# Optimization experiments

Measured on AMD Instinct MI355X. Metric: run time of the kernel, lower is better.

The kernel has to match this reference:

```python
import jax, jax.numpy as jnp
import numpy as np

N, E, D = 50000, 800000, 128
RESIDUAL_SCALE = 1.0
EPS = 1e-5  # torch LayerNorm default eps


def _mlp_ln(h, w1, b1, w2, b2, w3, b3, g, beta):
    # MeshGraphNets MLP: Linear -> SiLU -> Linear -> SiLU -> Linear -> LayerNorm
    h = jax.nn.silu(h @ w1 + b1)
    h = jax.nn.silu(h @ w2 + b2)
    h = h @ w3 + b3
    mu = h.mean(axis=-1, keepdims=True)
    var = ((h - mu) ** 2).mean(axis=-1, keepdims=True)
    return g * (h - mu) * jax.lax.rsqrt(var + EPS) + beta


def setup_inputs() -> dict:
    key = jax.random.key(0)
    ks = jax.random.split(key, 16)

    def lin(k, fan_in, fan_out):
        bound = 1.0 / np.sqrt(fan_in)
        kw, kb = jax.random.split(k)
        w = jax.random.uniform(kw, (fan_in, fan_out), jnp.float32, -bound, bound)
        b = jax.random.uniform(kb, (fan_out,), jnp.float32, -bound, bound)
        return w, b

    x = jax.random.normal(ks[0], (N, D), jnp.float32)
    edge_attr = jax.random.normal(ks[1], (E, D), jnp.float32)
    edge_index = jax.random.randint(ks[2], (2, E), 0, N, jnp.int32)

    ew1, eb1 = lin(ks[3], 3 * D, D)
    ew2, eb2 = lin(ks[4], D, D)
    ew3, eb3 = lin(ks[5], D, D)
    e_gamma = jnp.ones((D,), jnp.float32)
    e_beta = jnp.zeros((D,), jnp.float32)

    nw1, nb1 = lin(ks[6], 2 * D, D)
    nw2, nb2 = lin(ks[7], D, D)
    nw3, nb3 = lin(ks[8], D, D)
    n_gamma = jnp.ones((D,), jnp.float32)
    n_beta = jnp.zeros((D,), jnp.float32)

    return dict(x=x, edge_attr=edge_attr, edge_index=edge_index,
                ew1=ew1, eb1=eb1, ew2=ew2, eb2=eb2, ew3=ew3, eb3=eb3,
                e_gamma=e_gamma, e_beta=e_beta,
                nw1=nw1, nb1=nb1, nw2=nw2, nb2=nb2, nw3=nw3, nb3=nb3,
                n_gamma=n_gamma, n_beta=n_beta)


def reference(x, edge_attr, edge_index,
              ew1, eb1, ew2, eb2, ew3, eb3, e_gamma, e_beta,
              nw1, nb1, nw2, nb2, nw3, nb3, n_gamma, n_beta):
    senders, receivers = edge_index[0], edge_index[1]

    # EdgeBlock: gather endpoint node features, concat with edge_attr, MLP
    edge_in = jnp.concatenate([x[senders], x[receivers], edge_attr], axis=-1)  # [E, 3D]
    edge_mlp_out = _mlp_ln(edge_in, ew1, eb1, ew2, eb2, ew3, eb3, e_gamma, e_beta)  # [E, D]

    # NodeBlock: scatter-sum edge messages to receiver nodes, concat with x, MLP
    agg = jax.ops.segment_sum(edge_mlp_out, receivers, num_segments=N)  # [N, D]
    node_in = jnp.concatenate([x, agg], axis=-1)  # [N, 2D]
    node_mlp_out = _mlp_ln(node_in, nw1, nb1, nw2, nb2, nw3, nb3, n_gamma, n_beta)

    # Residual updates
    x_new = x + RESIDUAL_SCALE * node_mlp_out

    # PairNorm (use_pairnorm=True)
    x_centered = x_new - x_new.mean(axis=0, keepdims=True)
    rms = jnp.linalg.norm(x_centered) / jnp.sqrt(jnp.float32(x_new.shape[0])) + 1e-8
    x_new = x_centered / rms

    edge_attr_new = edge_attr + RESIDUAL_SCALE * edge_mlp_out
    return x_new, edge_attr_new
```

## Files before the change

### kernel.cpp

```cpp
#include <hip/hip_runtime.h>
#include <hip/hip_bf16.h>

#define NN 50000
#define NE 800000
#define ROWB 272

typedef unsigned short u16;
typedef unsigned int u32;
typedef __attribute__((ext_vector_type(4))) float f32x4;
typedef __attribute__((ext_vector_type(8))) short short8;


__device__ __forceinline__ u16 f2b(float f){ __hip_bfloat16 h = __float2bfloat16(f); u16 u; __builtin_memcpy(&u, &h, 2); return u; }
__device__ __forceinline__ float b2f(u16 u){ __hip_bfloat16 h; __builtin_memcpy(&h, &u, 2); return __bfloat162float(h); }
__device__ __forceinline__ float siluf(float v){ return v / (1.f + __expf(-v)); }

__device__ __forceinline__ uint4 cvt8(const float* __restrict__ s){
  const float4 a = *(const float4*)s;
  const float4 b = *(const float4*)(s + 4);
  union { u16 h[8]; uint4 q; } u;
  u.h[0]=f2b(a.x); u.h[1]=f2b(a.y); u.h[2]=f2b(a.z); u.h[3]=f2b(a.w);
  u.h[4]=f2b(b.x); u.h[5]=f2b(b.y); u.h[6]=f2b(b.z); u.h[7]=f2b(b.w);
  return u.q;
}

template<int K>
__device__ __forceinline__ void gemm128(f32x4 acc[4][2], const u16* __restrict__ sA,
                                        const u16* __restrict__ wB, int wm, int wn, int lane){
  const int l15 = lane & 15, l4 = lane >> 4;
  const u16* w0 = wB + (size_t)(wn*32 + l15)*K + l4*8;
  const u16* w1 = w0 + (size_t)16*K;
  #pragma unroll
  for (int ks = 0; ks < 4; ++ks){
    const short8 b0 = *(const short8*)(w0 + ks*32);
    const short8 b1 = *(const short8*)(w1 + ks*32);
    const int kb = ks*64 + l4*16;
    short8 a[4];
    #pragma unroll
    for (int fr = 0; fr < 4; ++fr)
      a[fr] = *(const short8*)((const char*)sA + (wm*64 + fr*16 + l15)*ROWB + kb);
    #pragma unroll
    for (int fr = 0; fr < 4; ++fr){
      acc[fr][0] = __builtin_amdgcn_mfma_f32_16x16x32_bf16(a[fr], b0, acc[fr][0], 0, 0, 0);
      acc[fr][1] = __builtin_amdgcn_mfma_f32_16x16x32_bf16(a[fr], b1, acc[fr][1], 0, 0, 0);
    }
  }
}

template<int K>
__device__ __forceinline__ void gemm64(f32x4 acc[2][4], const u16* __restrict__ sA,
                                       const u16* __restrict__ wB, int wm, int wn, int lane){
  const int l15 = lane & 15, l4 = lane >> 4;
  const u16* w0 = wB + (size_t)(wn*64 + l15)*K + l4*8;
  #pragma unroll
  for (int ks = 0; ks < 4; ++ks){
    short8 b[4];
    #pragma unroll
    for (int fc = 0; fc < 4; ++fc)
      b[fc] = *(const short8*)(w0 + (size_t)fc*16*K + ks*32);
    const int kb = ks*64 + l4*16;
    short8 a[2];
    #pragma unroll
    for (int fr = 0; fr < 2; ++fr)
      a[fr] = *(const short8*)((const char*)sA + (wm*32 + fr*16 + l15)*ROWB + kb);
    #pragma unroll
    for (int fr = 0; fr < 2; ++fr)
      #pragma unroll
      for (int fc = 0; fc < 4; ++fc)
        acc[fr][fc] = __builtin_amdgcn_mfma_f32_16x16x32_bf16(a[fr], b[fc], acc[fr][fc], 0, 0, 0);
  }
}

__device__ __forceinline__ void epilogue(const f32x4 acc[4][2], const float* __restrict__ bias,
                                         u16* __restrict__ dst, int wm, int wn, int lane, bool doSilu){
  const int l15 = lane & 15, l4 = lane >> 4;
  #pragma unroll
  for (int fc = 0; fc < 2; ++fc){
    const int col = wn*32 + fc*16 + l15;
    const float bv = bias[col];
    #pragma unroll
    for (int fr = 0; fr < 4; ++fr){
      const int rbase = wm*64 + fr*16 + l4*4;
      #pragma unroll
      for (int j = 0; j < 4; ++j){
        float v = acc[fr][fc][j] + bv;
        if (doSilu) v = siluf(v);
        *(u16*)((char*)dst + (rbase + j)*ROWB + col*2) = f2b(v);
      }
    }
  }
}

__global__ __launch_bounds__(256) void wtrans_kernel(const float* __restrict__ w1, const float* __restrict__ w2,
                                                     const float* __restrict__ w3, const float* __restrict__ m1,
                                                     const float* __restrict__ m2, const float* __restrict__ m3,
                                                     u16* __restrict__ wt){
  const int i = blockIdx.x * 256 + threadIdx.x;
  const float* src; int K, base, off;
  if      (i < 49152)  { src = w1; K = 384; base = 0;      off = i; }
  else if (i < 65536)  { src = w2; K = 128; base = 49152;  off = i - 49152; }
  else if (i < 81920)  { src = w3; K = 128; base = 65536;  off = i - 65536; }
  else if (i < 114688) { src = m1; K = 256; base = 81920;  off = i - 81920; }
  else if (i < 131072) { src = m2; K = 128; base = 114688; off = i - 114688; }
  else                 { src = m3; K = 128; base = 131072; off = i - 131072; }
  const int k = off >> 7, n = off & 127;
  wt[base + n*K + k] = f2b(src[off]);
}

__global__ __launch_bounds__(256) void prep_kernel(const float* __restrict__ x, u16* __restrict__ xB,
                                                   const int* __restrict__ eidx, int* __restrict__ cnt){
  const int i = blockIdx.x * 256 + threadIdx.x;
  if (xB){
    const size_t o = (size_t)i * 8;
    *(uint4*)(xB + o) = cvt8(x + o);
  }
  atomicAdd(&cnt[eidx[NE + i]], 1);
}

__global__ __launch_bounds__(1024) void scan_kernel(const int* __restrict__ cnt, int* __restrict__ off,
                                                    int* __restrict__ cursor){
  __shared__ int s[1024];
  const int t = threadIdx.x;
  const int CH = 49;
  int sum = 0;
  for (int i = 0; i < CH; ++i){
    const int idx = t*CH + i;
    if (idx < NN) sum += cnt[idx];
  }
  s[t] = sum;
  __syncthreads();
  for (int d = 1; d < 1024; d <<= 1){
    int v = (t >= d) ? s[t - d] : 0;
    __syncthreads();
    s[t] += v;
    __syncthreads();
  }
  int run = s[t] - sum;
  for (int i = 0; i < CH; ++i){
    const int idx = t*CH + i;
    if (idx < NN){
      off[idx] = run;
      cursor[idx] = run;
      run += cnt[idx];
      if (idx == NN - 1) off[NN] = run;
    }
  }
}

__global__ __launch_bounds__(256) void scatter_kernel(const int* __restrict__ eidx, int* __restrict__ cursor,
                                                      int* __restrict__ perm, int* __restrict__ slot){
  const int i = blockIdx.x * 256 + threadIdx.x;
  if (i < NE){
    const int pos = atomicAdd(&cursor[eidx[NE + i]], 1);
    perm[pos] = i;
    slot[i] = pos;
  }
}

__global__ __launch_bounds__(256, 4) void pre_kernel(const float* __restrict__ x, const u16* __restrict__ xB,
                                                     const u16* __restrict__ wt, u16* __restrict__ Pab){
  __shared__ u16 sX[64*136];
  const int t = threadIdx.x;
  const int nBase = blockIdx.x * 64;
  const int lane = t & 63, wid = t >> 6;
  const int wm = wid >> 1, wn = wid & 1;
  const int chunk = t & 15, r0 = t >> 4;

  #pragma unroll
  for (int p = 0; p < 4; ++p){
    const int row = r0 + p*16;
    const int node = nBase + row;
    uint4 v = {0u, 0u, 0u, 0u};
    if (node < NN){
      if (xB) v = *(const uint4*)(xB + (size_t)node*128 + chunk*8);
      else    v = cvt8(x + (size_t)node*128 + chunk*8);
    }
    *(uint4*)((char*)sX + row*ROWB + chunk*16) = v;
  }
  __syncthreads();

  const f32x4 z4 = {0.f, 0.f, 0.f, 0.f};
  const int l15 = lane & 15, l4 = lane >> 4;
  #pragma unroll
  for (int half = 0; half < 2; ++half){
    f32x4 acc[2][4];
    #pragma unroll
    for (int fr = 0; fr < 2; ++fr)
      #pragma unroll
      for (int fc = 0; fc < 4; ++fc) acc[fr][fc] = z4;
    gemm64<384>(acc, sX, wt + half*128, wm, wn, lane);
    #pragma unroll
    for (int fc = 0; fc < 4; ++fc){
      const int col = wn*64 + fc*16 + l15;
      #pragma unroll
      for (int fr = 0; fr < 2; ++fr){
        const int rbase = wm*32 + fr*16 + l4*4;
        #pragma unroll
        for (int j = 0; j < 4; ++j){
          const int node = nBase + rbase + j;
          if (node < NN) Pab[(size_t)node*256 + half*128 + col] = f2b(acc[fr][fc][j]);
        }
      }
    }
  }
}

__global__ __launch_bounds__(512, 4) void edge_kernel(
    const float* __restrict__ x, const u16* __restrict__ xB,
    const float* __restrict__ ea, const int* __restrict__ eidx,
    const u16* __restrict__ wt, const u16* __restrict__ Pab,
    const float* __restrict__ b1, const float* __restrict__ b2,
    const float* __restrict__ b3, const float* __restrict__ gma, const float* __restrict__ bta,
    const int* __restrict__ slot, float* __restrict__ outE, u16* __restrict__ oBuf)
{
  __shared__ u16 sA[128*136];
  __shared__ u16 sP[128*128];
  __shared__ float sMeta[640];
  __shared__ int sIdx[256];
  __shared__ int sSlot[128];
  const int t = threadIdx.x;
  const size_t eBase = (size_t)blockIdx.x * 128;

  if (t < 128){
    sIdx[t]       = eidx[eBase + t];
    sIdx[t + 128] = eidx[(size_t)NE + eBase + t];
    sSlot[t]      = slot[eBase + t];
    sMeta[t]       = b1[t];
    sMeta[t + 128] = b2[t];
    sMeta[t + 256] = b3[t];
    sMeta[t + 384] = gma[t];
    sMeta[t + 512] = bta[t];
  }
  __syncthreads();

  const int lane = t & 63, wid = t >> 6;
  const int wm = wid >> 2, wn = wid & 3;
  const int chunk = t & 15, r0 = t >> 4;

  const f32x4 z4 = {0.f, 0.f, 0.f, 0.f};
  f32x4 acc[4][2];
  #pragma unroll
  for (int fr = 0; fr < 4; ++fr){ acc[fr][0] = z4; acc[fr][1] = z4; }

  uint4 eaQ[4];

  #pragma unroll
  for (int p = 0; p < 4; ++p){
    const int row = r0 + p*32;
    uint4 v = cvt8(ea + ((eBase + row)*128 + chunk*8));
    eaQ[p] = v;
    *(uint4*)((char*)sA + row*ROWB + chunk*16) = v;
    const int sn = sIdx[row], rn = sIdx[row + 128];
    const uint4 qa = *(const uint4*)(Pab + (size_t)sn*256 + chunk*8);
    const uint4 qb = *(const uint4*)(Pab + (size_t)rn*256 + 128 + chunk*8);
    const u16* pa = (const u16*)&qa;
    const u16* pb = (const u16*)&qb;
    union { u16 h[8]; uint4 q; } u;
    #pragma unroll
    for (int j = 0; j < 8; ++j) u.h[j] = f2b(b2f(pa[j]) + b2f(pb[j]));
    *(uint4*)((char*)sP + row*256 + chunk*16) = u.q;
  }
  __syncthreads();
  gemm128<384>(acc, sA, wt + 256, wm, wn, lane);
  __syncthreads();

  {
    const int l15 = lane & 15, l4 = lane >> 4;
    #pragma unroll
    for (int fc = 0; fc < 2; ++fc){
      const int col = wn*32 + fc*16 + l15;
      const float bv = sMeta[col];
      #pragma unroll
      for (int fr = 0; fr < 4; ++fr){
        const int rbase = wm*64 + fr*16 + l4*4;
        #pragma unroll
        for (int j = 0; j < 4; ++j){
          const float pv = b2f(*(const u16*)((const char*)sP + (rbase + j)*256 + col*2));
          const float v = siluf(acc[fr][fc][j] + bv + pv);
          *(u16*)((char*)sA + (rbase + j)*ROWB + col*2) = f2b(v);
        }
      }
    }
  }
  __syncthreads();
  #pragma unroll
  for (int fr = 0; fr < 4; ++fr){ acc[fr][0] = z4; acc[fr][1] = z4; }
  gemm128<128>(acc, sA, wt + 49152, wm, wn, lane);
  __syncthreads();
  epilogue(acc, sMeta + 128, sA, wm, wn, lane, true);
  __syncthreads();
  #pragma unroll
  for (int fr = 0; fr < 4; ++fr){ acc[fr][0] = z4; acc[fr][1] = z4; }
  gemm128<128>(acc, sA, wt + 65536, wm, wn, lane);
  __syncthreads();
  epilogue(acc, sMeta + 256, sA, wm, wn, lane, false);
  __syncthreads();

  {
    #pragma unroll
    for (int p = 0; p < 4; ++p){
      const int row = r0 + p*32;
      uint4 q = *(const uint4*)((const char*)sA + row*ROWB + chunk*16);
      const u16* pu = (const u16*)&q;
      float h[8];
      #pragma unroll
      for (int j = 0; j < 8; ++j) h[j] = b2f(pu[j]);
      float s = 0.f;
      #pragma unroll
      for (int j = 0; j < 8; ++j) s += h[j];
      s += __shfl_xor(s, 1); s += __shfl_xor(s, 2); s += __shfl_xor(s, 4); s += __shfl_xor(s, 8);
      const float mu = s * (1.f/128.f);
      float ss = 0.f;
      #pragma unroll
      for (int j = 0; j < 8; ++j){ const float d = h[j] - mu; ss += d*d; }
      ss += __shfl_xor(ss, 1); ss += __shfl_xor(ss, 2); ss += __shfl_xor(ss, 4); ss += __shfl_xor(ss, 8);
      const float rs = rsqrtf(fmaxf(ss*(1.f/128.f), 0.f) + 1e-5f);
      const size_t e = eBase + row;
      const u16* ep = (const u16*)&eaQ[p];
      alignas(16) float orow[8];
      alignas(16) u16 obf[8];
      #pragma unroll
      for (int j = 0; j < 8; ++j){
        const int col = chunk*8 + j;
        const float o = sMeta[384 + col]*(h[j] - mu)*rs + sMeta[512 + col];
        orow[j] = b2f(ep[j]) + o;
        obf[j] = f2b(o);
      }
      float* dst = outE + e*128 + chunk*8;
      *(float4*)dst       = ((const float4*)orow)[0];
      *(float4*)(dst + 4) = ((const float4*)orow)[1];
      if (oBuf) *(uint4*)(oBuf + (size_t)sSlot[row]*128 + chunk*8) = *(const uint4*)obf;
    }
  }
}

__global__ __launch_bounds__(256) void agg_o_kernel(const u16* __restrict__ oBuf, const int* __restrict__ off,
                                                    float* __restrict__ agg){
  const int node = blockIdx.x * 4 + (threadIdx.x >> 6);
  const int lane = threadIdx.x & 63;
  if (node >= NN) return;
  const int s = off[node], e = off[node + 1];
  float a0 = 0.f, a1 = 0.f;
  for (int i = s; i < e; ++i){
    const u32 w = *(const u32*)(oBuf + (size_t)i*128 + lane*2);
    a0 += b2f((u16)(w & 0xFFFFu));
    a1 += b2f((u16)(w >> 16));
  }
  float2 r = {a0, a1};
  *(float2*)(agg + (size_t)node*128 + lane*2) = r;
}

__global__ __launch_bounds__(256) void agg_f_kernel(const float* __restrict__ outE, const float* __restrict__ ea,
                                                    const int* __restrict__ off, const int* __restrict__ perm,
                                                    float* __restrict__ agg){
  const int node = blockIdx.x * 4 + (threadIdx.x >> 6);
  const int lane = threadIdx.x & 63;
  if (node >= NN) return;
  const int s = off[node], e = off[node + 1];
  float a0 = 0.f, a1 = 0.f;
  for (int i = s; i < e; ++i){
    const size_t r = (size_t)perm[i] * 128;
    a0 += outE[r + lane]      - ea[r + lane];
    a1 += outE[r + 64 + lane] - ea[r + 64 + lane];
  }
  agg[(size_t)node*128 + lane]      = a0;
  agg[(size_t)node*128 + 64 + lane] = a1;
}

__global__ __launch_bounds__(512, 4) void node_kernel(
    const float* __restrict__ x, const float* __restrict__ agg, const u16* __restrict__ wt,
    const float* __restrict__ b1, const float* __restrict__ b2, const float* __restrict__ b3,
    const float* __restrict__ gma, const float* __restrict__ bta,
    float* __restrict__ outX, float* __restrict__ stats)
{
  __shared__ u16 sA[128*136];
  __shared__ float sMeta[640];
  __shared__ float sCol[128];
  __shared__ float sSq;
  const int t = threadIdx.x;
  const int nBase = blockIdx.x * 128;

  if (t < 128){
    sMeta[t]       = b1[t];
    sMeta[t + 128] = b2[t];
    sMeta[t + 256] = b3[t];
    sMeta[t + 384] = gma[t];
    sMeta[t + 512] = bta[t];
    sCol[t] = 0.f;
  }
  if (t == 0) sSq = 0.f;
  __syncthreads();

  const int lane = t & 63, wid = t >> 6;
  const int wm = wid >> 2, wn = wid & 3;
  const int chunk = t & 15, r0 = t >> 4;

  const f32x4 z4 = {0.f, 0.f, 0.f, 0.f};
  f32x4 acc[4][2];
  #pragma unroll
  for (int fr = 0; fr < 4; ++fr){ acc[fr][0] = z4; acc[fr][1] = z4; }

  for (int kc = 0; kc < 2; ++kc){
    #pragma unroll
    for (int p = 0; p < 4; ++p){
      const int row = r0 + p*32;
      const int node = nBase + row;
      uint4 v = {0u, 0u, 0u, 0u};
      if (node < NN){
        const float* s = (kc == 0) ? (x + (size_t)node*128 + chunk*8)
                                   : (agg + (size_t)node*128 + chunk*8);
        v = cvt8(s);
      }
      *(uint4*)((char*)sA + row*ROWB + chunk*16) = v;
    }
    __syncthreads();
    gemm128<256>(acc, sA, wt + 81920 + kc*128, wm, wn, lane);
    __syncthreads();
  }
  epilogue(acc, sMeta + 0, sA, wm, wn, lane, true);
  __syncthreads();
  #pragma unroll
  for (int fr = 0; fr < 4; ++fr){ acc[fr][0] = z4; acc[fr][1] = z4; }
  gemm128<128>(acc, sA, wt + 114688, wm, wn, lane);
  __syncthreads();
  epilogue(acc, sMeta + 128, sA, wm, wn, lane, true);
  __syncthreads();
  #pragma unroll
  for (int fr = 0; fr < 4; ++fr){ acc[fr][0] = z4; acc[fr][1] = z4; }
  gemm128<128>(acc, sA, wt + 131072, wm, wn, lane);
  __syncthreads();
  epilogue(acc, sMeta + 256, sA, wm, wn, lane, false);
  __syncthreads();

  {
    const int row = t >> 2, part = t & 3;
    const int node = nBase + row;
    float v[32];
    #pragma unroll
    for (int c = 0; c < 4; ++c){
      uint4 q = *(const uint4*)((const char*)sA + row*ROWB + part*64 + c*16);
      const u16* pu = (const u16*)&q;
      #pragma unroll
      for (int j = 0; j < 8; ++j) v[c*8 + j] = b2f(pu[j]);
    }
    float s = 0.f;
    #pragma unroll
    for (int i = 0; i < 32; ++i) s += v[i];
    s += __shfl_xor(s, 1);  s += __shfl_xor(s, 2);
    const float mu = s * (1.f/128.f);
    float ss = 0.f;
    #pragma unroll
    for (int i = 0; i < 32; ++i){ const float d = v[i] - mu; ss += d*d; }
    ss += __shfl_xor(ss, 1);  ss += __shfl_xor(ss, 2);
    const float rs = rsqrtf(fmaxf(ss*(1.f/128.f), 0.f) + 1e-5f);
    float lssq = 0.f;
    if (node < NN){
      const float* xRow = x + (size_t)node*128 + part*32;
      alignas(16) float orow[32];
      #pragma unroll
      for (int i = 0; i < 32; ++i){
        const int col = part*32 + i;
        const float o = sMeta[384 + col]*(v[i] - mu)*rs + sMeta[512 + col];
        const float res = xRow[i] + o;
        orow[i] = res;
        atomicAdd(&sCol[col], res);
        lssq += res*res;
      }
      float* dst = outX + (size_t)node*128 + part*32;
      #pragma unroll
      for (int c = 0; c < 8; ++c) *(float4*)(dst + c*4) = ((const float4*)orow)[c];
    }
    #pragma unroll
    for (int m = 1; m < 64; m <<= 1) lssq += __shfl_xor(lssq, m);
    if (lane == 0) atomicAdd(&sSq, lssq);
  }
  __syncthreads();
  if (t < 128) atomicAdd(&stats[t], sCol[t]);
  if (t == 0)  atomicAdd(&stats[128], sSq);
}

__global__ __launch_bounds__(256) void pairnorm_kernel(float* __restrict__ xOut, const float* __restrict__ stats){
  __shared__ float sMean[128];
  __shared__ float sP2[2];
  __shared__ float sInv;
  const int t = threadIdx.x;
  float m2 = 0.f;
  if (t < 128){
    const float mean = stats[t] * (1.f / (float)NN);
    sMean[t] = mean;
    m2 = mean * mean;
  }
  #pragma unroll
  for (int m = 1; m < 64; m <<= 1) m2 += __shfl_xor(m2, m);
  if ((t & 63) == 0 && t < 128) sP2[t >> 6] = m2;
  __syncthreads();
  if (t == 0){
    float ssc = stats[128] - (float)NN * (sP2[0] + sP2[1]);
    ssc = fmaxf(ssc, 0.f);
    const float rms = sqrtf(ssc * (1.f / (float)NN)) + 1e-8f;
    sInv = 1.f / rms;
  }
  __syncthreads();
  const size_t base = ((size_t)blockIdx.x * 256 + t) * 4;
  const int col = (int)(base & 127);
  float4 q = *(float4*)(xOut + base);
  const float inv = sInv;
  q.x = (q.x - sMean[col])     * inv;
  q.y = (q.y - sMean[col + 1]) * inv;
  q.z = (q.z - sMean[col + 2]) * inv;
  q.w = (q.w - sMean[col + 3]) * inv;
  *(float4*)(xOut + base) = q;
}

extern "C" void kernel_launch(void* const* d_in, const int* in_sizes, int n_in,
                              void* d_out, int out_size, void* d_ws, size_t ws_size,
                              hipStream_t stream){
  (void)in_sizes; (void)n_in; (void)out_size;
  const float* x    = (const float*)d_in[0];
  const float* ea   = (const float*)d_in[1];
  const int*   eidx = (const int*)d_in[2];
  const float* ew1  = (const float*)d_in[3];
  const float* eb1  = (const float*)d_in[4];
  const float* ew2  = (const float*)d_in[5];
  const float* eb2  = (const float*)d_in[6];
  const float* ew3  = (const float*)d_in[7];
  const float* eb3  = (const float*)d_in[8];
  const float* eg   = (const float*)d_in[9];
  const float* ebt  = (const float*)d_in[10];
  const float* nw1  = (const float*)d_in[11];
  const float* nb1  = (const float*)d_in[12];
  const float* nw2  = (const float*)d_in[13];
  const float* nb2  = (const float*)d_in[14];
  const float* nw3  = (const float*)d_in[15];
  const float* nb3  = (const float*)d_in[16];
  const float* ng   = (const float*)d_in[17];
  const float* nbt  = (const float*)d_in[18];

  u16*   wt     = (u16*)d_ws;
  float* stats  = (float*)((char*)d_ws + 294912);
  int*   cnt    = (int*)((char*)d_ws + 297216);
  int*   off    = (int*)((char*)d_ws + 497408);
  int*   cursor = (int*)((char*)d_ws + 697600);
  int*   perm   = (int*)((char*)d_ws + 897792);
  int*   slot   = (int*)((char*)d_ws + 4097792);
  const bool useO = ws_size >= (7297792ull + (size_t)NE * 128 * 2);
  const bool useX = ws_size >= (7297792ull + (size_t)NE * 128 * 2 + (size_t)NN * 128 * 2);
  u16*   oBuf   = useO ? (u16*)((char*)d_ws + 7297792) : (u16*)nullptr;
  u16*   xB     = useX ? (u16*)((char*)d_ws + 7297792 + (size_t)NE * 128 * 2) : (u16*)nullptr;
  float* outX   = (float*)d_out;
  u16*   Pab    = (u16*)d_out;
  float* outE   = outX + (size_t)NN * 128;

  hipMemsetAsync(stats, 0, 2048, stream);
  hipMemsetAsync(cnt, 0, NN * sizeof(int), stream);
  wtrans_kernel<<<576, 256, 0, stream>>>(ew1, ew2, ew3, nw1, nw2, nw3, wt);
  prep_kernel<<<3125, 256, 0, stream>>>(x, xB, eidx, cnt);
  scan_kernel<<<1, 1024, 0, stream>>>(cnt, off, cursor);
  scatter_kernel<<<3125, 256, 0, stream>>>(eidx, cursor, perm, slot);
  pre_kernel<<<782, 256, 0, stream>>>(x, xB, wt, Pab);
  edge_kernel<<<6250, 512, 0, stream>>>(x, xB, ea, eidx, wt, Pab, eb1, eb2, eb3, eg, ebt, slot, outE, oBuf);
  if (useO) agg_o_kernel<<<12500, 256, 0, stream>>>(oBuf, off, outX);
  else      agg_f_kernel<<<12500, 256, 0, stream>>>(outE, ea, off, perm, outX);
  node_kernel<<<391, 512, 0, stream>>>(x, outX, wt, nb1, nb2, nb3, ng, nbt, outX, stats);
  pairnorm_kernel<<<6250, 256, 0, stream>>>(outX, stats);
}
```

Measured before the change: 792.7 us.

## Fuse weight transpose into prep, seed edge GEMM accumulators, fuse aggregation into node kernel

```diff
diff --git a/kernel.cpp b/kernel.cpp
--- a/kernel.cpp
+++ b/kernel.cpp
@@ -91,25 +91,24 @@
   }
 }
 
-__global__ __launch_bounds__(256) void wtrans_kernel(const float* __restrict__ w1, const float* __restrict__ w2,
-                                                     const float* __restrict__ w3, const float* __restrict__ m1,
-                                                     const float* __restrict__ m2, const float* __restrict__ m3,
-                                                     u16* __restrict__ wt){
-  const int i = blockIdx.x * 256 + threadIdx.x;
-  const float* src; int K, base, off;
-  if      (i < 49152)  { src = w1; K = 384; base = 0;      off = i; }
-  else if (i < 65536)  { src = w2; K = 128; base = 49152;  off = i - 49152; }
-  else if (i < 81920)  { src = w3; K = 128; base = 65536;  off = i - 65536; }
-  else if (i < 114688) { src = m1; K = 256; base = 81920;  off = i - 81920; }
-  else if (i < 131072) { src = m2; K = 128; base = 114688; off = i - 114688; }
-  else                 { src = m3; K = 128; base = 131072; off = i - 131072; }
-  const int k = off >> 7, n = off & 127;
-  wt[base + n*K + k] = f2b(src[off]);
-}
-
-__global__ __launch_bounds__(256) void prep_kernel(const float* __restrict__ x, u16* __restrict__ xB,
+__global__ __launch_bounds__(256) void prep_kernel(const float* __restrict__ w1, const float* __restrict__ w2,
+                                                   const float* __restrict__ w3, const float* __restrict__ m1,
+                                                   const float* __restrict__ m2, const float* __restrict__ m3,
+                                                   u16* __restrict__ wt,
+                                                   const float* __restrict__ x, u16* __restrict__ xB,
                                                    const int* __restrict__ eidx, int* __restrict__ cnt){
   const int i = blockIdx.x * 256 + threadIdx.x;
+  if (i < 147456){
+    const float* src; int K, base, off;
+    if      (i < 49152)  { src = w1; K = 384; base = 0;      off = i; }
+    else if (i < 65536)  { src = w2; K = 128; base = 49152;  off = i - 49152; }
+    else if (i < 81920)  { src = w3; K = 128; base = 65536;  off = i - 65536; }
+    else if (i < 114688) { src = m1; K = 256; base = 81920;  off = i - 81920; }
+    else if (i < 131072) { src = m2; K = 128; base = 114688; off = i - 114688; }
+    else                 { src = m3; K = 128; base = 131072; off = i - 131072; }
+    const int k = off >> 7, n = off & 127;
+    wt[base + n*K + k] = f2b(src[off]);
+  }
   if (xB){
     const size_t o = (size_t)i * 8;
     *(uint4*)(xB + o) = cvt8(x + o);
@@ -205,8 +204,7 @@
   }
 }
 
-__global__ __launch_bounds__(512, 4) void edge_kernel(
-    const float* __restrict__ x, const u16* __restrict__ xB,
+__global__ __launch_bounds__(512, 6) void edge_kernel(
     const float* __restrict__ ea, const int* __restrict__ eidx,
     const u16* __restrict__ wt, const u16* __restrict__ Pab,
     const float* __restrict__ b1, const float* __restrict__ b2,
@@ -214,7 +212,6 @@
     const int* __restrict__ slot, float* __restrict__ outE, u16* __restrict__ oBuf)
 {
   __shared__ u16 sA[128*136];
-  __shared__ u16 sP[128*128];
   __shared__ float sMeta[640];
   __shared__ int sIdx[256];
   __shared__ int sSlot[128];
@@ -236,20 +233,11 @@
   const int lane = t & 63, wid = t >> 6;
   const int wm = wid >> 2, wn = wid & 3;
   const int chunk = t & 15, r0 = t >> 4;
-
-  const f32x4 z4 = {0.f, 0.f, 0.f, 0.f};
-  f32x4 acc[4][2];
-  #pragma unroll
-  for (int fr = 0; fr < 4; ++fr){ acc[fr][0] = z4; acc[fr][1] = z4; }
-
-  uint4 eaQ[4];
+  const int l15 = lane & 15, l4 = lane >> 4;
 
   #pragma unroll
   for (int p = 0; p < 4; ++p){
     const int row = r0 + p*32;
-    uint4 v = cvt8(ea + ((eBase + row)*128 + chunk*8));
-    eaQ[p] = v;
-    *(uint4*)((char*)sA + row*ROWB + chunk*16) = v;
     const int sn = sIdx[row], rn = sIdx[row + 128];
     const uint4 qa = *(const uint4*)(Pab + (size_t)sn*256 + chunk*8);
     const uint4 qb = *(const uint4*)(Pab + (size_t)rn*256 + 128 + chunk*8);
@@ -258,31 +246,36 @@
     union { u16 h[8]; uint4 q; } u;
     #pragma unroll
     for (int j = 0; j < 8; ++j) u.h[j] = f2b(b2f(pa[j]) + b2f(pb[j]));
-    *(uint4*)((char*)sP + row*256 + chunk*16) = u.q;
-  }
-  __syncthreads();
-  gemm128<384>(acc, sA, wt + 256, wm, wn, lane);
-  __syncthreads();
-
-  {
-    const int l15 = lane & 15, l4 = lane >> 4;
+    *(uint4*)((char*)sA + row*ROWB + chunk*16) = u.q;
+  }
+  __syncthreads();
+
+  f32x4 acc[4][2];
+  #pragma unroll
+  for (int fr = 0; fr < 4; ++fr)
     #pragma unroll
     for (int fc = 0; fc < 2; ++fc){
       const int col = wn*32 + fc*16 + l15;
-      const float bv = sMeta[col];
-      #pragma unroll
-      for (int fr = 0; fr < 4; ++fr){
-        const int rbase = wm*64 + fr*16 + l4*4;
-        #pragma unroll
-        for (int j = 0; j < 4; ++j){
-          const float pv = b2f(*(const u16*)((const char*)sP + (rbase + j)*256 + col*2));
-          const float v = siluf(acc[fr][fc][j] + bv + pv);
-          *(u16*)((char*)sA + (rbase + j)*ROWB + col*2) = f2b(v);
-        }
-      }
-    }
-  }
-  __syncthreads();
+      #pragma unroll
+      for (int j = 0; j < 4; ++j)
+        acc[fr][fc][j] = b2f(*(const u16*)((const char*)sA + (wm*64 + fr*16 + l4*4 + j)*ROWB + col*2));
+    }
+  __syncthreads();
+
+  uint4 eaQ[4];
+  #pragma unroll
+  for (int p = 0; p < 4; ++p){
+    const int row = r0 + p*32;
+    uint4 v = cvt8(ea + ((eBase + row)*128 + chunk*8));
+    eaQ[p] = v;
+    *(uint4*)((char*)sA + row*ROWB + chunk*16) = v;
+  }
+  __syncthreads();
+  gemm128<384>(acc, sA, wt + 256, wm, wn, lane);
+  __syncthreads();
+  epilogue(acc, sMeta + 0, sA, wm, wn, lane, true);
+  __syncthreads();
+  const f32x4 z4 = {0.f, 0.f, 0.f, 0.f};
   #pragma unroll
   for (int fr = 0; fr < 4; ++fr){ acc[fr][0] = z4; acc[fr][1] = z4; }
   gemm128<128>(acc, sA, wt + 49152, wm, wn, lane);
@@ -332,22 +325,6 @@
       if (oBuf) *(uint4*)(oBuf + (size_t)sSlot[row]*128 + chunk*8) = *(const uint4*)obf;
     }
   }
-}
-
-__global__ __launch_bounds__(256) void agg_o_kernel(const u16* __restrict__ oBuf, const int* __restrict__ off,
-                                                    float* __restrict__ agg){
-  const int node = blockIdx.x * 4 + (threadIdx.x >> 6);
-  const int lane = threadIdx.x & 63;
-  if (node >= NN) return;
-  const int s = off[node], e = off[node + 1];
-  float a0 = 0.f, a1 = 0.f;
-  for (int i = s; i < e; ++i){
-    const u32 w = *(const u32*)(oBuf + (size_t)i*128 + lane*2);
-    a0 += b2f((u16)(w & 0xFFFFu));
-    a1 += b2f((u16)(w >> 16));
-  }
-  float2 r = {a0, a1};
-  *(float2*)(agg + (size_t)node*128 + lane*2) = r;
 }
 
 __global__ __launch_bounds__(256) void agg_f_kernel(const float* __restrict__ outE, const float* __restrict__ ea,
@@ -368,7 +345,9 @@
 }
 
 __global__ __launch_bounds__(512, 4) void node_kernel(
-    const float* __restrict__ x, const float* __restrict__ agg, const u16* __restrict__ wt,
+    const float* __restrict__ x, const float* __restrict__ aggF,
+    const u16* __restrict__ oBuf, const int* __restrict__ off,
+    const u16* __restrict__ wt,
     const float* __restrict__ b1, const float* __restrict__ b2, const float* __restrict__ b3,
     const float* __restrict__ gma, const float* __restrict__ bta,
     float* __restrict__ outX, float* __restrict__ stats)
@@ -407,9 +386,24 @@
       const int node = nBase + row;
       uint4 v = {0u, 0u, 0u, 0u};
       if (node < NN){
-        const float* s = (kc == 0) ? (x + (size_t)node*128 + chunk*8)
-                                   : (agg + (size_t)node*128 + chunk*8);
-        v = cvt8(s);
+        if (kc == 0){
+          v = cvt8(x + (size_t)node*128 + chunk*8);
+        } else if (oBuf){
+          float a[8] = {0.f,0.f,0.f,0.f,0.f,0.f,0.f,0.f};
+          const int s0 = off[node], e0 = off[node + 1];
+          for (int i = s0; i < e0; ++i){
+            uint4 q = *(const uint4*)(oBuf + (size_t)i*128 + chunk*8);
+            const u16* pu = (const u16*)&q;
+            #pragma unroll
+            for (int j = 0; j < 8; ++j) a[j] += b2f(pu[j]);
+          }
+          union { u16 h[8]; uint4 q; } u;
+          #pragma unroll
+          for (int j = 0; j < 8; ++j) u.h[j] = f2b(a[j]);
+          v = u.q;
+        } else {
+          v = cvt8(aggF + (size_t)node*128 + chunk*8);
+        }
       }
       *(uint4*)((char*)sA + row*ROWB + chunk*16) = v;
     }
@@ -553,14 +547,12 @@
 
   hipMemsetAsync(stats, 0, 2048, stream);
   hipMemsetAsync(cnt, 0, NN * sizeof(int), stream);
-  wtrans_kernel<<<576, 256, 0, stream>>>(ew1, ew2, ew3, nw1, nw2, nw3, wt);
-  prep_kernel<<<3125, 256, 0, stream>>>(x, xB, eidx, cnt);
+  prep_kernel<<<3125, 256, 0, stream>>>(ew1, ew2, ew3, nw1, nw2, nw3, wt, x, xB, eidx, cnt);
   scan_kernel<<<1, 1024, 0, stream>>>(cnt, off, cursor);
   scatter_kernel<<<3125, 256, 0, stream>>>(eidx, cursor, perm, slot);
   pre_kernel<<<782, 256, 0, stream>>>(x, xB, wt, Pab);
-  edge_kernel<<<6250, 512, 0, stream>>>(x, xB, ea, eidx, wt, Pab, eb1, eb2, eb3, eg, ebt, slot, outE, oBuf);
-  if (useO) agg_o_kernel<<<12500, 256, 0, stream>>>(oBuf, off, outX);
-  else      agg_f_kernel<<<12500, 256, 0, stream>>>(outE, ea, off, perm, outX);
-  node_kernel<<<391, 512, 0, stream>>>(x, outX, wt, nb1, nb2, nb3, ng, nbt, outX, stats);
+  edge_kernel<<<6250, 512, 0, stream>>>(ea, eidx, wt, Pab, eb1, eb2, eb3, eg, ebt, slot, outE, oBuf);
+  if (!useO) agg_f_kernel<<<12500, 256, 0, stream>>>(outE, ea, off, perm, outX);
+  node_kernel<<<391, 512, 0, stream>>>(x, outX, oBuf, off, wt, nb1, nb2, nb3, ng, nbt, outX, stats);
   pairnorm_kernel<<<6250, 256, 0, stream>>>(outX, stats);
 }
```

New measurement: 858.4 us. +8.3%, slower.
